# Kernel tuning notes

Measured on AMD Instinct MI355X. Metric: run time of the kernel, lower is better.

Reference implementation:

```python
import jax, jax.numpy as jnp
import numpy as np


def setup_inputs() -> dict:
    key = jax.random.key(0)
    ks = jax.random.split(key, 8)
    B, N, E, D, C = 64, 1024, 16384, 1024, 128
    x = jax.random.normal(ks[0], (B, D), dtype=jnp.float32)
    edge_index = jax.random.randint(ks[1], (2, E), 0, N, dtype=jnp.int64)
    W_emb = jax.random.normal(ks[2], (D, C), dtype=jnp.float32) * (2.0 / D) ** 0.5
    b_emb = jnp.zeros((C,), dtype=jnp.float32)
    W_conv = jax.random.normal(ks[3], (C, C), dtype=jnp.float32) * (2.0 / C) ** 0.5
    b_conv = jnp.zeros((C,), dtype=jnp.float32)
    W_cls = jax.random.normal(ks[4], (C, 1), dtype=jnp.float32) * (2.0 / C) ** 0.5
    b_cls = jnp.zeros((1,), dtype=jnp.float32)
    return {"x": x, "edge_index": edge_index, "W_emb": W_emb, "b_emb": b_emb,
            "W_conv": W_conv, "b_conv": b_conv, "W_cls": W_cls, "b_cls": b_cls,
            "n_nodes": N, "n_conv": 4}


def reference(x, edge_index, W_emb, b_emb, W_conv, b_conv, W_cls, b_cls, n_nodes, n_conv):
    B = x.shape[0]
    total = B * n_nodes
    # tile each flattened sample across all nodes of its graph copy  [B*N, D]
    x_batch = jnp.repeat(x.reshape(B, -1), n_nodes, axis=0)
    # batched edge index: disjoint union of B copies of the graph  [2, B*E]
    offs = (jnp.arange(B, dtype=edge_index.dtype) * n_nodes)[None, :, None]
    ei = (edge_index[:, None, :] + offs).reshape(2, -1)
    src, dst = ei[0], ei[1]
    # embedding: Linear + ReLU
    h = jax.nn.relu(x_batch @ W_emb + b_emb)
    # n_conv applications of the SAME GCNConv (no self loops, no normalization) + ReLU
    def conv(h, _):
        hw = h @ W_conv                                   # [B*N, C]
        agg = jax.ops.segment_sum(hw[src], dst, num_segments=total)
        return jax.nn.relu(agg + b_conv), None
    h, _ = jax.lax.scan(conv, h, None, length=n_conv)
    # node 0 of each graph copy, then classifier
    out = h[::n_nodes] @ W_cls + b_cls                    # [B, 1]
    return out
```

## Files before the change

kernel.cpp:

```cpp
#include <hip/hip_runtime.h>
#include <cstdint>
#include <cstddef>

constexpr int Bn = 64;
constexpr int Nn = 1024;
constexpr int Dn = 1024;
constexpr int Cn = 128;
constexpr int En = 16384;
constexpr int DMAX = 64;
constexpr int NB3 = 192;

typedef short s16x8 __attribute__((ext_vector_type(8)));
typedef float f32x4 __attribute__((ext_vector_type(4)));

__device__ __forceinline__ uint32_t f2bf(float f) {
    uint32_t u = __float_as_uint(f);
    return (u + 0x7fffu + ((u >> 16) & 1u)) >> 16;
}

__global__ __launch_bounds__(256) void k_prep(const float* __restrict__ x,
                                              const float* __restrict__ We,
                                              const float* __restrict__ Wc,
                                              const int* __restrict__ ei32,
                                              float* __restrict__ pws,
                                              unsigned short* __restrict__ Wt,
                                              unsigned int* __restrict__ epk,
                                              int* __restrict__ hists,
                                              int* __restrict__ f3,
                                              int* __restrict__ Mm,
                                              int* __restrict__ n3cur,
                                              int* __restrict__ meta) {
    int bid = blockIdx.x, tid = threadIdx.x;
    if (bid < 512) {
        __shared__ float sx[128];
        __shared__ float sp[256];
        int b = bid >> 3, q = bid & 7;
        int c = tid & 127, h = tid >> 7;
        if (tid < 128) sx[tid] = x[b * Dn + q * 128 + tid];
        __syncthreads();
        float acc = 0.f;
        int kl = h * 64;
        int d0 = q * 128 + kl;
#pragma unroll 8
        for (int i = 0; i < 64; ++i) acc += sx[kl + i] * We[(d0 + i) * Cn + c];
        sp[h * 128 + c] = acc;
        __syncthreads();
        if (h == 0) pws[(b * 8 + q) * Cn + c] = sp[c] + sp[128 + c];
    } else if (bid < 576) {
        int i = (bid - 512) * 256 + tid;
        int n = i >> 7, k = i & 127;
        Wt[i] = (unsigned short)f2bf(Wc[k * Cn + n]);
    } else if (bid < 592) {
        int hb = bid - 576;
        __shared__ int hloc[Nn];
        __shared__ int det;
#pragma unroll
        for (int r = 0; r < 4; ++r) hloc[r * 256 + tid] = 0;
        if (tid == 0) det = 0;
        __syncthreads();
        int base = hb * 1024;
        int hw = 0;
#pragma unroll
        for (int r = 0; r < 4; ++r) { int i = base + r * 256 + tid; hw |= ei32[2 * i + 1]; }
        if (hw) atomicOr(&det, 1);
        __syncthreads();
        bool i64 = (det == 0);
#pragma unroll
        for (int r = 0; r < 4; ++r) {
            int i = base + r * 256 + tid;
            int s, d;
            if (i64) {
                s = ((const int2*)ei32)[i].x & (Nn - 1);
                d = ((const int2*)ei32)[En + i].x & (Nn - 1);
            } else {
                s = ei32[i] & (Nn - 1);
                d = ei32[En + i] & (Nn - 1);
            }
            epk[i] = (unsigned)s | ((unsigned)d << 16);
            atomicAdd(&hloc[d], 1);
            if (d == 0) f3[s] = 1;
        }
        __syncthreads();
#pragma unroll
        for (int r = 0; r < 4; ++r) hists[hb * Nn + r * 256 + tid] = hloc[r * 256 + tid];
    } else if (bid < 596) {
        int4 z = {0, 0, 0, 0};
        int4* M4 = (int4*)Mm;
#pragma unroll
        for (int r = 0; r < 16; ++r) M4[(bid - 592) * 4096 + r * 256 + tid] = z;
    } else {
        int4 z = {0, 0, 0, 0};
        ((int4*)n3cur)[tid] = z;
        if (tid == 0) meta[4] = 0;
    }
}

__global__ __launch_bounds__(1024) void k_build(const int* __restrict__ hists,
                                                const unsigned int* __restrict__ epk,
                                                const int* __restrict__ f3,
                                                int* __restrict__ f2,
                                                int* __restrict__ Mm,
                                                int* __restrict__ n3cur,
                                                int* __restrict__ n3src,
                                                int* __restrict__ e0,
                                                int* __restrict__ L3,
                                                int* __restrict__ meta,
                                                const float* __restrict__ pws,
                                                const float* __restrict__ be,
                                                const float* __restrict__ Wc,
                                                float* __restrict__ g) {
    int bid = blockIdx.x, t = threadIdx.x;
    if (bid < 16) {
        __shared__ int sInd[Nn];
        int v = 0;
#pragma unroll
        for (int h = 0; h < 16; ++h) v += hists[h * Nn + t];
        sInd[t] = v;
        __syncthreads();
        unsigned e = epk[bid * 1024 + t];
        int s = e & 0xffff, d = e >> 16;
        int dd = sInd[s]; if (dd > DMAX - 1) dd = DMAX - 1;
        atomicAdd(&Mm[d * DMAX + dd], 1);
        if (f3[d] == 1) {
            f2[s] = 1;
            int p = atomicAdd(&n3cur[d], 1);
            if (p < NB3) n3src[d * NB3 + p] = s;
        }
        if (d == 0) {
            int p = atomicAdd(&meta[4], 1);
            if (p < 1024) e0[p] = s;
        }
    } else if (bid == 16) {
        __shared__ int c3;
        if (t == 0) c3 = 0;
        __syncthreads();
        if (f3[t] == 1) { int p = atomicAdd(&c3, 1); L3[p] = t; }
        __syncthreads();
        if (t == 0) meta[2] = c3;
    } else {
        __shared__ float se[8][Cn];
        int blk = bid - 17, bi = t >> 7, c = t & 127, b = blk * 8 + bi;
        float e4 = be[c];
#pragma unroll
        for (int q = 0; q < 8; ++q) e4 += pws[(b * 8 + q) * Cn + c];
        se[bi][c] = fmaxf(e4, 0.f);
        __syncthreads();
        float acc = 0.f;
#pragma unroll 8
        for (int k = 0; k < Cn; ++k) acc += se[bi][k] * Wc[k * Cn + c];
        g[b * Cn + c] = acc;
    }
}

constexpr int PAD = 136;
constexpr int PADR = 72;

__global__ __launch_bounds__(256, 4) void k_conv2M(const float* __restrict__ g,
                                                   float* __restrict__ h2,
                                                   const unsigned short* __restrict__ Wt,
                                                   const float* __restrict__ bc,
                                                   const int* __restrict__ Mm,
                                                   const int* __restrict__ f2) {
    int bidx = blockIdx.x;
    int tile0 = bidx >> 6, b = bidx & 63;
    __shared__ int sL2[Nn];
    __shared__ int sWs[4];
    __shared__ unsigned short sRt[128 * PADR];
    __shared__ unsigned short sMb[32 * PADR];
    __shared__ unsigned short sSb[32 * PAD];
    __shared__ int snode[32];
    int tid = threadIdx.x, lane = tid & 63, w = tid >> 6;
    int m = lane & 15, quad = lane >> 4;

    int n0 = tid * 4;
    int fl0 = (f2[n0] == 1), fl1 = (f2[n0 + 1] == 1), fl2 = (f2[n0 + 2] == 1), fl3 = (f2[n0 + 3] == 1);
    int c = fl0 + fl1 + fl2 + fl3;
    int inc = c;
    for (int off = 1; off < 64; off <<= 1) {
        int nv = __shfl_up(inc, off);
        if (lane >= off) inc += nv;
    }
    if (lane == 63) sWs[w] = inc;
    __syncthreads();
    int wbase = 0;
#pragma unroll
    for (int q = 0; q < 4; ++q) wbase += (q < w) ? sWs[q] : 0;
    int cnt2 = sWs[0] + sWs[1] + sWs[2] + sWs[3];
    int pos = wbase + inc - c;
    if (fl0) sL2[pos++] = n0;
    if (fl1) sL2[pos++] = n0 + 1;
    if (fl2) sL2[pos++] = n0 + 2;
    if (fl3) sL2[pos++] = n0 + 3;

    {
        int cc = tid & 127, dh = tid >> 7;
        float gc = g[b * Cn + cc], bcc = bc[cc];
#pragma unroll
        for (int d = dh * 32; d < dh * 32 + 32; ++d) {
            float r = fmaxf(fmaf((float)d, gc, bcc), 0.f);
            sRt[cc * PADR + d] = (unsigned short)f2bf(r);
        }
    }

    s16x8 bf0[4], bf1[4];
#pragma unroll
    for (int ks = 0; ks < 4; ++ks) {
        int ko = ks * 32 + quad * 8;
        bf0[ks] = *(const s16x8*)&Wt[(w * 32 + m) * Cn + ko];
        bf1[ks] = *(const s16x8*)&Wt[(w * 32 + 16 + m) * Cn + ko];
    }
    __syncthreads();

    for (int tile = tile0; tile * 32 < cnt2; tile += 8) {
        __syncthreads();
        if (tid < 32) {
            int ti = tile * 32 + tid;
            snode[tid] = (ti < cnt2) ? sL2[ti] : -1;
        }
        __syncthreads();
        {
            int row = tid >> 3, seg = tid & 7;
            int node = snode[row];
            unsigned short pk[8];
            if (node >= 0) {
                const int4* mp = (const int4*)&Mm[node * DMAX + seg * 8];
                int4 a = mp[0], bq = mp[1];
                pk[0] = (unsigned short)f2bf((float)a.x);
                pk[1] = (unsigned short)f2bf((float)a.y);
                pk[2] = (unsigned short)f2bf((float)a.z);
                pk[3] = (unsigned short)f2bf((float)a.w);
                pk[4] = (unsigned short)f2bf((float)bq.x);
                pk[5] = (unsigned short)f2bf((float)bq.y);
                pk[6] = (unsigned short)f2bf((float)bq.z);
                pk[7] = (unsigned short)f2bf((float)bq.w);
            } else {
#pragma unroll
                for (int i = 0; i < 8; ++i) pk[i] = 0;
            }
            *(uint4*)&sMb[row * PADR + seg * 8] = *(uint4*)pk;
        }
        __syncthreads();

        f32x4 acc1[2][2];
#pragma unroll
        for (int rt = 0; rt < 2; ++rt)
#pragma unroll
            for (int ct = 0; ct < 2; ++ct) acc1[rt][ct] = (f32x4){0.f, 0.f, 0.f, 0.f};
#pragma unroll
        for (int ks = 0; ks < 2; ++ks) {
            int ko = ks * 32 + quad * 8;
            s16x8 a0 = *(const s16x8*)&sMb[m * PADR + ko];
            s16x8 a1 = *(const s16x8*)&sMb[(16 + m) * PADR + ko];
            s16x8 r0 = *(const s16x8*)&sRt[(w * 32 + m) * PADR + ko];
            s16x8 r1 = *(const s16x8*)&sRt[(w * 32 + 16 + m) * PADR + ko];
            acc1[0][0] = __builtin_amdgcn_mfma_f32_16x16x32_bf16(a0, r0, acc1[0][0], 0, 0, 0);
            acc1[0][1] = __builtin_amdgcn_mfma_f32_16x16x32_bf16(a0, r1, acc1[0][1], 0, 0, 0);
            acc1[1][0] = __builtin_amdgcn_mfma_f32_16x16x32_bf16(a1, r0, acc1[1][0], 0, 0, 0);
            acc1[1][1] = __builtin_amdgcn_mfma_f32_16x16x32_bf16(a1, r1, acc1[1][1], 0, 0, 0);
        }
#pragma unroll
        for (int rt = 0; rt < 2; ++rt)
#pragma unroll
            for (int ct = 0; ct < 2; ++ct) {
                int col = w * 32 + ct * 16 + m;
#pragma unroll
                for (int reg = 0; reg < 4; ++reg) {
                    int row = rt * 16 + quad * 4 + reg;
                    sSb[row * PAD + col] = (unsigned short)f2bf(acc1[rt][ct][reg]);
                }
            }
        __syncthreads();

        f32x4 acc[2][2];
#pragma unroll
        for (int rt = 0; rt < 2; ++rt)
#pragma unroll
            for (int ct = 0; ct < 2; ++ct) acc[rt][ct] = (f32x4){0.f, 0.f, 0.f, 0.f};
#pragma unroll
        for (int ks = 0; ks < 4; ++ks) {
            int ko = ks * 32 + quad * 8;
            s16x8 a0 = *(const s16x8*)&sSb[(0 * 16 + m) * PAD + ko];
            s16x8 a1 = *(const s16x8*)&sSb[(1 * 16 + m) * PAD + ko];
            acc[0][0] = __builtin_amdgcn_mfma_f32_16x16x32_bf16(a0, bf0[ks], acc[0][0], 0, 0, 0);
            acc[0][1] = __builtin_amdgcn_mfma_f32_16x16x32_bf16(a0, bf1[ks], acc[0][1], 0, 0, 0);
            acc[1][0] = __builtin_amdgcn_mfma_f32_16x16x32_bf16(a1, bf0[ks], acc[1][0], 0, 0, 0);
            acc[1][1] = __builtin_amdgcn_mfma_f32_16x16x32_bf16(a1, bf1[ks], acc[1][1], 0, 0, 0);
        }

#pragma unroll
        for (int rt = 0; rt < 2; ++rt)
#pragma unroll
            for (int ct = 0; ct < 2; ++ct) {
                int col = w * 32 + ct * 16 + m;
                float bias = bc[col];
#pragma unroll
                for (int reg = 0; reg < 4; ++reg) {
                    int row = rt * 16 + quad * 4 + reg;
                    int node = snode[row];
                    if (node >= 0)
                        h2[((size_t)b * Nn + node) * Cn + col] = fmaxf(acc[rt][ct][reg] + bias, 0.f);
                }
            }
    }
}

__global__ __launch_bounds__(256) void k_conv34(const float* __restrict__ h2,
                                                const unsigned short* __restrict__ Wt,
                                                const float* __restrict__ bc,
                                                const int* __restrict__ L3,
                                                const int* __restrict__ meta,
                                                const int* __restrict__ n3cur,
                                                const int* __restrict__ n3src,
                                                const int* __restrict__ e0,
                                                const float* __restrict__ Wc,
                                                const float* __restrict__ Wcls,
                                                const float* __restrict__ bcls,
                                                float* __restrict__ out) {
    __shared__ unsigned short sSb[32 * PAD];
    __shared__ int sIdx[32][64];
    __shared__ float sH3[32][Cn];
    __shared__ short smap[Nn];
    __shared__ int snode[32], scnt[32];
    __shared__ float sAgg[8][Cn];
    __shared__ float sred[256];
    __shared__ int sI[256];
    int b = blockIdx.x, tid = threadIdx.x;
    int cnt3 = meta[2];
    int m0 = meta[4]; if (m0 > 1024) m0 = 1024;
    int lim = m0 < 256 ? m0 : 256;
    if (tid < lim) sI[tid] = e0[tid];

    int w = tid >> 6, lane = tid & 63, m = lane & 15, quad = lane >> 4;
    s16x8 bf0[4], bf1[4];
#pragma unroll
    for (int ks = 0; ks < 4; ++ks) {
        int ko = ks * 32 + quad * 8;
        bf0[ks] = *(const s16x8*)&Wt[(w * 32 + m) * Cn + ko];
        bf1[ks] = *(const s16x8*)&Wt[(w * 32 + 16 + m) * Cn + ko];
    }
    int c4 = tid & 31, u = tid >> 5;
    const float4* hb4 = (const float4*)(h2 + (size_t)b * (Nn * Cn));
    float4 aAgg = {0.f, 0.f, 0.f, 0.f};

    for (int tile = 0; tile * 32 < cnt3; ++tile) {
        __syncthreads();
#pragma unroll
        for (int r = 0; r < 4; ++r) smap[tid + 256 * r] = -1;
        if (tid < 32) {
            int ti = tile * 32 + tid;
            int node = (ti < cnt3) ? L3[ti] : -1;
            snode[tid] = node;
            int cnt = (node >= 0) ? n3cur[node] : 0;
            if (cnt > NB3) cnt = NB3;
            scnt[tid] = cnt;
        }
        __syncthreads();
        if (tid < 32 && snode[tid] >= 0) smap[snode[tid]] = (short)tid;
#pragma unroll
        for (int r = 0; r < 8; ++r) {
            int row = w * 8 + r;
            int cnt = scnt[row];
            if (lane < cnt && lane < 64) sIdx[row][lane] = n3src[snode[row] * NB3 + lane];
        }
        __syncthreads();

#pragma unroll
        for (int t0 = 0; t0 < 4; ++t0) {
            int row = u * 4 + t0;
            int cnt = scnt[row];
            float4 a = {0.f, 0.f, 0.f, 0.f};
            int jm = cnt < 64 ? cnt : 64;
            for (int j = 0; j < jm; ++j) {
                float4 v = hb4[sIdx[row][j] * 32 + c4];
                a.x += v.x; a.y += v.y; a.z += v.z; a.w += v.w;
            }
            for (int j = 64; j < cnt; ++j) {
                float4 v = hb4[n3src[snode[row] * NB3 + j] * 32 + c4];
                a.x += v.x; a.y += v.y; a.z += v.z; a.w += v.w;
            }
            uint2 pk;
            pk.x = f2bf(a.x) | (f2bf(a.y) << 16);
            pk.y = f2bf(a.z) | (f2bf(a.w) << 16);
            *(uint2*)&sSb[row * PAD + c4 * 4] = pk;
        }
        __syncthreads();

        f32x4 acc[2][2];
#pragma unroll
        for (int rt = 0; rt < 2; ++rt)
#pragma unroll
            for (int ct = 0; ct < 2; ++ct) acc[rt][ct] = (f32x4){0.f, 0.f, 0.f, 0.f};
#pragma unroll
        for (int ks = 0; ks < 4; ++ks) {
            int ko = ks * 32 + quad * 8;
            s16x8 a0 = *(const s16x8*)&sSb[(0 * 16 + m) * PAD + ko];
            s16x8 a1 = *(const s16x8*)&sSb[(1 * 16 + m) * PAD + ko];
            acc[0][0] = __builtin_amdgcn_mfma_f32_16x16x32_bf16(a0, bf0[ks], acc[0][0], 0, 0, 0);
            acc[0][1] = __builtin_amdgcn_mfma_f32_16x16x32_bf16(a0, bf1[ks], acc[0][1], 0, 0, 0);
            acc[1][0] = __builtin_amdgcn_mfma_f32_16x16x32_bf16(a1, bf0[ks], acc[1][0], 0, 0, 0);
            acc[1][1] = __builtin_amdgcn_mfma_f32_16x16x32_bf16(a1, bf1[ks], acc[1][1], 0, 0, 0);
        }

#pragma unroll
        for (int rt = 0; rt < 2; ++rt)
#pragma unroll
            for (int ct = 0; ct < 2; ++ct) {
                int col = w * 32 + ct * 16 + m;
                float bias = bc[col];
#pragma unroll
                for (int reg = 0; reg < 4; ++reg) {
                    int row = rt * 16 + quad * 4 + reg;
                    sH3[row][col] = fmaxf(acc[rt][ct][reg] + bias, 0.f);
                }
            }
        __syncthreads();

        for (int j = u; j < lim; j += 8) {
            int r2 = smap[sI[j]];
            if (r2 >= 0) {
                float4 v = *(const float4*)&sH3[r2][c4 * 4];
                aAgg.x += v.x; aAgg.y += v.y; aAgg.z += v.z; aAgg.w += v.w;
            }
        }
        for (int j = 256 + u; j < m0; j += 8) {
            int r2 = smap[e0[j]];
            if (r2 >= 0) {
                float4 v = *(const float4*)&sH3[r2][c4 * 4];
                aAgg.x += v.x; aAgg.y += v.y; aAgg.z += v.z; aAgg.w += v.w;
            }
        }
    }

    *(float4*)&sAgg[u][c4 * 4] = aAgg;
    __syncthreads();
    int c = tid & 127, half = tid >> 7;
    if (tid < 128) {
        float s = sAgg[0][c];
#pragma unroll
        for (int q2 = 1; q2 < 8; ++q2) s += sAgg[q2][c];
        sAgg[0][c] = s;
    }
    __syncthreads();
    float s = 0.f;
    int k0 = half * 64;
#pragma unroll 8
    for (int k = k0; k < k0 + 64; ++k) s += sAgg[0][k] * Wc[k * Cn + c];
    sred[tid] = s;
    __syncthreads();
    if (tid < 128) {
        float val = fmaxf(sred[c] + sred[128 + c] + bc[c], 0.f);
        sred[tid] = val * Wcls[c];
    }
    __syncthreads();
    for (int st = 64; st > 0; st >>= 1) {
        if (tid < st) sred[tid] += sred[tid + st];
        __syncthreads();
    }
    if (tid == 0) out[b] = sred[0] + bcls[0];
}

extern "C" void kernel_launch(void* const* d_in, const int* in_sizes, int n_in,
                              void* d_out, int out_size, void* d_ws, size_t ws_size,
                              hipStream_t stream) {
    const float* x    = (const float*)d_in[0];
    const int*   ei32 = (const int*)d_in[1];
    const float* We   = (const float*)d_in[2];
    const float* be   = (const float*)d_in[3];
    const float* Wc   = (const float*)d_in[4];
    const float* bc   = (const float*)d_in[5];
    const float* Wcls = (const float*)d_in[6];
    const float* bcls = (const float*)d_in[7];
    float* out = (float*)d_out;

    char* ws = (char*)d_ws;
    float*          g      = (float*)(ws + 0);
    int*            meta   = (int*)(ws + 32768);
    int*            e0     = (int*)(ws + 36864);
    int*            n3cur  = (int*)(ws + 40960);
    unsigned short* Wt     = (unsigned short*)(ws + 45056);
    float*          pws    = (float*)(ws + 77824);
    int*            f3     = (int*)(ws + 339968);
    int*            f2     = (int*)(ws + 344064);
    unsigned int*   epk    = (unsigned int*)(ws + 348160);
    int*            hists  = (int*)(ws + 413696);
    int*            Mm     = (int*)(ws + 479232);
    int*            n3src  = (int*)(ws + 741376);
    int*            L3     = (int*)(ws + 1527808);
    float*          h2full = (float*)(ws + 1531904);

    k_prep<<<597, 256, 0, stream>>>(x, We, Wc, ei32, pws, Wt, epk, hists, f3, Mm, n3cur, meta);
    k_build<<<25, 1024, 0, stream>>>(hists, epk, f3, f2, Mm, n3cur, n3src, e0, L3, meta,
                                     pws, be, Wc, g);
    k_conv2M<<<8 * Bn, 256, 0, stream>>>(g, h2full, Wt, bc, Mm, f2);
    k_conv34<<<Bn, 256, 0, stream>>>(h2full, Wt, bc, L3, meta, n3cur, n3src, e0,
                                     Wc, Wcls, bcls, out);
}
```

Measured before the change: 109.3 us.

## Fuse build, conv2 and conv3/4 kernels into one persistent kernel with global flags

Merges the graph-build, second-conv and final conv/classifier kernels into a single launch of 576 blocks. Blocks coordinate through global atomic counters and acquire spin-waits on a sync counter and per-batch h2 completion counters. Each conv2 block now recomputes its own embedding-times-W_conv vector, so the separate g stage is no longer needed. This removes two kernel launch boundaries and their drain gaps, but it relies on all 576 blocks being co-resident to avoid deadlock and adds spin-wait and fence overhead.

```diff
diff --git a/kernel.cpp b/kernel.cpp
--- a/kernel.cpp
+++ b/kernel.cpp
@@ -91,372 +91,404 @@
     } else {
         int4 z = {0, 0, 0, 0};
         ((int4*)n3cur)[tid] = z;
-        if (tid == 0) meta[4] = 0;
+        if (tid < 64) ((int4*)meta)[tid] = z;
     }
 }
 
-__global__ __launch_bounds__(1024) void k_build(const int* __restrict__ hists,
-                                                const unsigned int* __restrict__ epk,
-                                                const int* __restrict__ f3,
-                                                int* __restrict__ f2,
-                                                int* __restrict__ Mm,
-                                                int* __restrict__ n3cur,
-                                                int* __restrict__ n3src,
-                                                int* __restrict__ e0,
-                                                int* __restrict__ L3,
-                                                int* __restrict__ meta,
-                                                const float* __restrict__ pws,
-                                                const float* __restrict__ be,
-                                                const float* __restrict__ Wc,
-                                                float* __restrict__ g) {
-    int bid = blockIdx.x, t = threadIdx.x;
-    if (bid < 16) {
-        __shared__ int sInd[Nn];
-        int v = 0;
-#pragma unroll
-        for (int h = 0; h < 16; ++h) v += hists[h * Nn + t];
-        sInd[t] = v;
-        __syncthreads();
-        unsigned e = epk[bid * 1024 + t];
-        int s = e & 0xffff, d = e >> 16;
-        int dd = sInd[s]; if (dd > DMAX - 1) dd = DMAX - 1;
-        atomicAdd(&Mm[d * DMAX + dd], 1);
-        if (f3[d] == 1) {
-            f2[s] = 1;
-            int p = atomicAdd(&n3cur[d], 1);
-            if (p < NB3) n3src[d * NB3 + p] = s;
-        }
-        if (d == 0) {
-            int p = atomicAdd(&meta[4], 1);
-            if (p < 1024) e0[p] = s;
-        }
-    } else if (bid == 16) {
-        __shared__ int c3;
-        if (t == 0) c3 = 0;
-        __syncthreads();
-        if (f3[t] == 1) { int p = atomicAdd(&c3, 1); L3[p] = t; }
-        __syncthreads();
-        if (t == 0) meta[2] = c3;
-    } else {
-        __shared__ float se[8][Cn];
-        int blk = bid - 17, bi = t >> 7, c = t & 127, b = blk * 8 + bi;
-        float e4 = be[c];
-#pragma unroll
-        for (int q = 0; q < 8; ++q) e4 += pws[(b * 8 + q) * Cn + c];
-        se[bi][c] = fmaxf(e4, 0.f);
-        __syncthreads();
-        float acc = 0.f;
-#pragma unroll 8
-        for (int k = 0; k < Cn; ++k) acc += se[bi][k] * Wc[k * Cn + c];
-        g[b * Cn + c] = acc;
-    }
-}
-
 constexpr int PAD = 136;
 constexpr int PADR = 72;
 
-__global__ __launch_bounds__(256, 4) void k_conv2M(const float* __restrict__ g,
-                                                   float* __restrict__ h2,
-                                                   const unsigned short* __restrict__ Wt,
-                                                   const float* __restrict__ bc,
-                                                   const int* __restrict__ Mm,
-                                                   const int* __restrict__ f2) {
-    int bidx = blockIdx.x;
-    int tile0 = bidx >> 6, b = bidx & 63;
-    __shared__ int sL2[Nn];
-    __shared__ int sWs[4];
-    __shared__ unsigned short sRt[128 * PADR];
-    __shared__ unsigned short sMb[32 * PADR];
-    __shared__ unsigned short sSb[32 * PAD];
-    __shared__ int snode[32];
-    int tid = threadIdx.x, lane = tid & 63, w = tid >> 6;
-    int m = lane & 15, quad = lane >> 4;
-
-    int n0 = tid * 4;
-    int fl0 = (f2[n0] == 1), fl1 = (f2[n0 + 1] == 1), fl2 = (f2[n0 + 2] == 1), fl3 = (f2[n0 + 3] == 1);
-    int c = fl0 + fl1 + fl2 + fl3;
-    int inc = c;
-    for (int off = 1; off < 64; off <<= 1) {
-        int nv = __shfl_up(inc, off);
-        if (lane >= off) inc += nv;
-    }
-    if (lane == 63) sWs[w] = inc;
-    __syncthreads();
-    int wbase = 0;
-#pragma unroll
-    for (int q = 0; q < 4; ++q) wbase += (q < w) ? sWs[q] : 0;
-    int cnt2 = sWs[0] + sWs[1] + sWs[2] + sWs[3];
-    int pos = wbase + inc - c;
-    if (fl0) sL2[pos++] = n0;
-    if (fl1) sL2[pos++] = n0 + 1;
-    if (fl2) sL2[pos++] = n0 + 2;
-    if (fl3) sL2[pos++] = n0 + 3;
-
-    {
-        int cc = tid & 127, dh = tid >> 7;
-        float gc = g[b * Cn + cc], bcc = bc[cc];
-#pragma unroll
-        for (int d = dh * 32; d < dh * 32 + 32; ++d) {
-            float r = fmaxf(fmaf((float)d, gc, bcc), 0.f);
-            sRt[cc * PADR + d] = (unsigned short)f2bf(r);
-        }
-    }
-
-    s16x8 bf0[4], bf1[4];
-#pragma unroll
-    for (int ks = 0; ks < 4; ++ks) {
-        int ko = ks * 32 + quad * 8;
-        bf0[ks] = *(const s16x8*)&Wt[(w * 32 + m) * Cn + ko];
-        bf1[ks] = *(const s16x8*)&Wt[(w * 32 + 16 + m) * Cn + ko];
-    }
-    __syncthreads();
-
-    for (int tile = tile0; tile * 32 < cnt2; tile += 8) {
-        __syncthreads();
-        if (tid < 32) {
-            int ti = tile * 32 + tid;
-            snode[tid] = (ti < cnt2) ? sL2[ti] : -1;
+__global__ __launch_bounds__(256, 3) void k_fused(const float* __restrict__ pws,
+                                                  const float* __restrict__ be,
+                                                  const float* __restrict__ Wc,
+                                                  const float* __restrict__ bc,
+                                                  const unsigned short* __restrict__ Wt,
+                                                  const int* __restrict__ f3,
+                                                  int* __restrict__ f2,
+                                                  const unsigned int* __restrict__ epk,
+                                                  const int* __restrict__ hists,
+                                                  int* __restrict__ Mm,
+                                                  int* __restrict__ n3cur,
+                                                  int* __restrict__ n3src,
+                                                  int* __restrict__ e0,
+                                                  int* __restrict__ L3,
+                                                  int* __restrict__ meta,
+                                                  float* __restrict__ h2,
+                                                  const float* __restrict__ Wcls,
+                                                  const float* __restrict__ bcls,
+                                                  float* __restrict__ out) {
+    __shared__ char smem[43776];
+    __shared__ int sMisc[2];
+    int bid = blockIdx.x, tid = threadIdx.x;
+    int lane = tid & 63, w = tid >> 6, m = lane & 15, quad = lane >> 4;
+    int* sync0  = &meta[8];
+    int* h2done = &meta[64];
+
+    if (bid < 512) {
+        int tile0 = bid >> 6, b = bid & 63;
+        int*   shInt = (int*)smem;
+        int*   sWs   = (int*)(smem + 4096);
+        float* sE    = (float*)(smem + 4112);
+        float* sGp   = (float*)(smem + 4624);
+        float* sG    = (float*)(smem + 5648);
+        int*   snode = (int*)(smem + 6160);
+        unsigned short* sRt = (unsigned short*)(smem + 6400);
+        unsigned short* sMb = (unsigned short*)(smem + 24832);
+        unsigned short* sSb = (unsigned short*)(smem + 29440);
+
+        if (bid < 16) {
+            for (int i = tid; i < Nn; i += 256) {
+                int v = 0;
+#pragma unroll
+                for (int h = 0; h < 16; ++h) v += hists[h * Nn + i];
+                shInt[i] = v;
+            }
+            __syncthreads();
+#pragma unroll
+            for (int r = 0; r < 4; ++r) {
+                unsigned e = epk[bid * 1024 + r * 256 + tid];
+                int s = e & 0xffff, d = e >> 16;
+                int dd = shInt[s]; if (dd > DMAX - 1) dd = DMAX - 1;
+                atomicAdd(&Mm[d * DMAX + dd], 1);
+                if (f3[d] == 1) {
+                    f2[s] = 1;
+                    int p = atomicAdd(&n3cur[d], 1);
+                    if (p < NB3) n3src[d * NB3 + p] = s;
+                }
+                if (d == 0) {
+                    int p = atomicAdd(&meta[4], 1);
+                    if (p < 1024) e0[p] = s;
+                }
+            }
+            __threadfence();
+            __syncthreads();
+            if (tid == 0)
+                __hip_atomic_fetch_add(sync0, 1, __ATOMIC_RELEASE, __HIP_MEMORY_SCOPE_AGENT);
+            __syncthreads();
+        } else if (bid == 16) {
+            if (tid == 0) sMisc[0] = 0;
+            __syncthreads();
+            for (int i = tid; i < Nn; i += 256)
+                if (f3[i] == 1) { int p = atomicAdd(&sMisc[0], 1); L3[p] = i; }
+            __syncthreads();
+            if (tid == 0) meta[2] = sMisc[0];
+            __threadfence();
+            __syncthreads();
+            if (tid == 0)
+                __hip_atomic_fetch_add(sync0, 1, __ATOMIC_RELEASE, __HIP_MEMORY_SCOPE_AGENT);
+            __syncthreads();
+        }
+
+        int cc = tid & 127, half = tid >> 7;
+        if (half == 0) {
+            float e4 = be[cc];
+#pragma unroll
+            for (int q = 0; q < 8; ++q) e4 += pws[(b * 8 + q) * Cn + cc];
+            sE[cc] = fmaxf(e4, 0.f);
         }
         __syncthreads();
         {
-            int row = tid >> 3, seg = tid & 7;
-            int node = snode[row];
-            unsigned short pk[8];
-            if (node >= 0) {
-                const int4* mp = (const int4*)&Mm[node * DMAX + seg * 8];
-                int4 a = mp[0], bq = mp[1];
-                pk[0] = (unsigned short)f2bf((float)a.x);
-                pk[1] = (unsigned short)f2bf((float)a.y);
-                pk[2] = (unsigned short)f2bf((float)a.z);
-                pk[3] = (unsigned short)f2bf((float)a.w);
-                pk[4] = (unsigned short)f2bf((float)bq.x);
-                pk[5] = (unsigned short)f2bf((float)bq.y);
-                pk[6] = (unsigned short)f2bf((float)bq.z);
-                pk[7] = (unsigned short)f2bf((float)bq.w);
-            } else {
-#pragma unroll
-                for (int i = 0; i < 8; ++i) pk[i] = 0;
-            }
-            *(uint4*)&sMb[row * PADR + seg * 8] = *(uint4*)pk;
-        }
-        __syncthreads();
-
-        f32x4 acc1[2][2];
-#pragma unroll
-        for (int rt = 0; rt < 2; ++rt)
-#pragma unroll
-            for (int ct = 0; ct < 2; ++ct) acc1[rt][ct] = (f32x4){0.f, 0.f, 0.f, 0.f};
-#pragma unroll
-        for (int ks = 0; ks < 2; ++ks) {
-            int ko = ks * 32 + quad * 8;
-            s16x8 a0 = *(const s16x8*)&sMb[m * PADR + ko];
-            s16x8 a1 = *(const s16x8*)&sMb[(16 + m) * PADR + ko];
-            s16x8 r0 = *(const s16x8*)&sRt[(w * 32 + m) * PADR + ko];
-            s16x8 r1 = *(const s16x8*)&sRt[(w * 32 + 16 + m) * PADR + ko];
-            acc1[0][0] = __builtin_amdgcn_mfma_f32_16x16x32_bf16(a0, r0, acc1[0][0], 0, 0, 0);
-            acc1[0][1] = __builtin_amdgcn_mfma_f32_16x16x32_bf16(a0, r1, acc1[0][1], 0, 0, 0);
-            acc1[1][0] = __builtin_amdgcn_mfma_f32_16x16x32_bf16(a1, r0, acc1[1][0], 0, 0, 0);
-            acc1[1][1] = __builtin_amdgcn_mfma_f32_16x16x32_bf16(a1, r1, acc1[1][1], 0, 0, 0);
-        }
-#pragma unroll
-        for (int rt = 0; rt < 2; ++rt)
-#pragma unroll
-            for (int ct = 0; ct < 2; ++ct) {
-                int col = w * 32 + ct * 16 + m;
-#pragma unroll
-                for (int reg = 0; reg < 4; ++reg) {
-                    int row = rt * 16 + quad * 4 + reg;
-                    sSb[row * PAD + col] = (unsigned short)f2bf(acc1[rt][ct][reg]);
-                }
-            }
-        __syncthreads();
-
-        f32x4 acc[2][2];
-#pragma unroll
-        for (int rt = 0; rt < 2; ++rt)
-#pragma unroll
-            for (int ct = 0; ct < 2; ++ct) acc[rt][ct] = (f32x4){0.f, 0.f, 0.f, 0.f};
+            float gp = 0.f;
+            int k0 = half * 64;
+#pragma unroll 8
+            for (int k = k0; k < k0 + 64; ++k) gp += sE[k] * Wc[k * Cn + cc];
+            sGp[half * 128 + cc] = gp;
+        }
+        __syncthreads();
+        if (half == 0) sG[cc] = sGp[cc] + sGp[128 + cc];
+        __syncthreads();
+
+        {
+            float gc = sG[cc], bcc = bc[cc];
+#pragma unroll
+            for (int d = half * 32; d < half * 32 + 32; ++d) {
+                float r = fmaxf(fmaf((float)d, gc, bcc), 0.f);
+                sRt[cc * PADR + d] = (unsigned short)f2bf(r);
+            }
+        }
+
+        s16x8 bf0[4], bf1[4];
 #pragma unroll
         for (int ks = 0; ks < 4; ++ks) {
             int ko = ks * 32 + quad * 8;
-            s16x8 a0 = *(const s16x8*)&sSb[(0 * 16 + m) * PAD + ko];
-            s16x8 a1 = *(const s16x8*)&sSb[(1 * 16 + m) * PAD + ko];
-            acc[0][0] = __builtin_amdgcn_mfma_f32_16x16x32_bf16(a0, bf0[ks], acc[0][0], 0, 0, 0);
-            acc[0][1] = __builtin_amdgcn_mfma_f32_16x16x32_bf16(a0, bf1[ks], acc[0][1], 0, 0, 0);
-            acc[1][0] = __builtin_amdgcn_mfma_f32_16x16x32_bf16(a1, bf0[ks], acc[1][0], 0, 0, 0);
-            acc[1][1] = __builtin_amdgcn_mfma_f32_16x16x32_bf16(a1, bf1[ks], acc[1][1], 0, 0, 0);
-        }
-
-#pragma unroll
-        for (int rt = 0; rt < 2; ++rt)
-#pragma unroll
-            for (int ct = 0; ct < 2; ++ct) {
-                int col = w * 32 + ct * 16 + m;
-                float bias = bc[col];
-#pragma unroll
-                for (int reg = 0; reg < 4; ++reg) {
-                    int row = rt * 16 + quad * 4 + reg;
-                    int node = snode[row];
-                    if (node >= 0)
-                        h2[((size_t)b * Nn + node) * Cn + col] = fmaxf(acc[rt][ct][reg] + bias, 0.f);
-                }
-            }
-    }
-}
-
-__global__ __launch_bounds__(256) void k_conv34(const float* __restrict__ h2,
-                                                const unsigned short* __restrict__ Wt,
-                                                const float* __restrict__ bc,
-                                                const int* __restrict__ L3,
-                                                const int* __restrict__ meta,
-                                                const int* __restrict__ n3cur,
-                                                const int* __restrict__ n3src,
-                                                const int* __restrict__ e0,
-                                                const float* __restrict__ Wc,
-                                                const float* __restrict__ Wcls,
-                                                const float* __restrict__ bcls,
-                                                float* __restrict__ out) {
-    __shared__ unsigned short sSb[32 * PAD];
-    __shared__ int sIdx[32][64];
-    __shared__ float sH3[32][Cn];
-    __shared__ short smap[Nn];
-    __shared__ int snode[32], scnt[32];
-    __shared__ float sAgg[8][Cn];
-    __shared__ float sred[256];
-    __shared__ int sI[256];
-    int b = blockIdx.x, tid = threadIdx.x;
-    int cnt3 = meta[2];
-    int m0 = meta[4]; if (m0 > 1024) m0 = 1024;
-    int lim = m0 < 256 ? m0 : 256;
-    if (tid < lim) sI[tid] = e0[tid];
-
-    int w = tid >> 6, lane = tid & 63, m = lane & 15, quad = lane >> 4;
-    s16x8 bf0[4], bf1[4];
-#pragma unroll
-    for (int ks = 0; ks < 4; ++ks) {
-        int ko = ks * 32 + quad * 8;
-        bf0[ks] = *(const s16x8*)&Wt[(w * 32 + m) * Cn + ko];
-        bf1[ks] = *(const s16x8*)&Wt[(w * 32 + 16 + m) * Cn + ko];
-    }
-    int c4 = tid & 31, u = tid >> 5;
-    const float4* hb4 = (const float4*)(h2 + (size_t)b * (Nn * Cn));
-    float4 aAgg = {0.f, 0.f, 0.f, 0.f};
-
-    for (int tile = 0; tile * 32 < cnt3; ++tile) {
-        __syncthreads();
-#pragma unroll
-        for (int r = 0; r < 4; ++r) smap[tid + 256 * r] = -1;
-        if (tid < 32) {
-            int ti = tile * 32 + tid;
-            int node = (ti < cnt3) ? L3[ti] : -1;
-            snode[tid] = node;
-            int cnt = (node >= 0) ? n3cur[node] : 0;
-            if (cnt > NB3) cnt = NB3;
-            scnt[tid] = cnt;
-        }
-        __syncthreads();
-        if (tid < 32 && snode[tid] >= 0) smap[snode[tid]] = (short)tid;
-#pragma unroll
-        for (int r = 0; r < 8; ++r) {
-            int row = w * 8 + r;
-            int cnt = scnt[row];
-            if (lane < cnt && lane < 64) sIdx[row][lane] = n3src[snode[row] * NB3 + lane];
-        }
-        __syncthreads();
-
-#pragma unroll
-        for (int t0 = 0; t0 < 4; ++t0) {
-            int row = u * 4 + t0;
-            int cnt = scnt[row];
-            float4 a = {0.f, 0.f, 0.f, 0.f};
-            int jm = cnt < 64 ? cnt : 64;
-            for (int j = 0; j < jm; ++j) {
-                float4 v = hb4[sIdx[row][j] * 32 + c4];
-                a.x += v.x; a.y += v.y; a.z += v.z; a.w += v.w;
-            }
-            for (int j = 64; j < cnt; ++j) {
-                float4 v = hb4[n3src[snode[row] * NB3 + j] * 32 + c4];
-                a.x += v.x; a.y += v.y; a.z += v.z; a.w += v.w;
-            }
-            uint2 pk;
-            pk.x = f2bf(a.x) | (f2bf(a.y) << 16);
-            pk.y = f2bf(a.z) | (f2bf(a.w) << 16);
-            *(uint2*)&sSb[row * PAD + c4 * 4] = pk;
-        }
-        __syncthreads();
-
-        f32x4 acc[2][2];
-#pragma unroll
-        for (int rt = 0; rt < 2; ++rt)
-#pragma unroll
-            for (int ct = 0; ct < 2; ++ct) acc[rt][ct] = (f32x4){0.f, 0.f, 0.f, 0.f};
+            bf0[ks] = *(const s16x8*)&Wt[(w * 32 + m) * Cn + ko];
+            bf1[ks] = *(const s16x8*)&Wt[(w * 32 + 16 + m) * Cn + ko];
+        }
+
+        if (tid == 0) {
+            while (__hip_atomic_load(sync0, __ATOMIC_ACQUIRE, __HIP_MEMORY_SCOPE_AGENT) < 17)
+                __builtin_amdgcn_s_sleep(2);
+        }
+        __syncthreads();
+
+        int n0 = tid * 4;
+        int fl0 = (f2[n0] == 1), fl1 = (f2[n0 + 1] == 1),
+            fl2 = (f2[n0 + 2] == 1), fl3 = (f2[n0 + 3] == 1);
+        int cflags = fl0 + fl1 + fl2 + fl3;
+        int inc = cflags;
+        for (int off = 1; off < 64; off <<= 1) {
+            int nv = __shfl_up(inc, off);
+            if (lane >= off) inc += nv;
+        }
+        if (lane == 63) sWs[w] = inc;
+        __syncthreads();
+        int wbase = 0;
+#pragma unroll
+        for (int q = 0; q < 4; ++q) wbase += (q < w) ? sWs[q] : 0;
+        int cnt2 = sWs[0] + sWs[1] + sWs[2] + sWs[3];
+        int pos = wbase + inc - cflags;
+        if (fl0) shInt[pos++] = n0;
+        if (fl1) shInt[pos++] = n0 + 1;
+        if (fl2) shInt[pos++] = n0 + 2;
+        if (fl3) shInt[pos++] = n0 + 3;
+
+        for (int tile = tile0; tile * 32 < cnt2; tile += 8) {
+            __syncthreads();
+            if (tid < 32) {
+                int ti = tile * 32 + tid;
+                snode[tid] = (ti < cnt2) ? shInt[ti] : -1;
+            }
+            __syncthreads();
+            {
+                int row = tid >> 3, seg = tid & 7;
+                int node = snode[row];
+                unsigned short pk[8];
+                if (node >= 0) {
+                    const int4* mp = (const int4*)&Mm[node * DMAX + seg * 8];
+                    int4 a = mp[0], bq = mp[1];
+                    pk[0] = (unsigned short)f2bf((float)a.x);
+                    pk[1] = (unsigned short)f2bf((float)a.y);
+                    pk[2] = (unsigned short)f2bf((float)a.z);
+                    pk[3] = (unsigned short)f2bf((float)a.w);
+                    pk[4] = (unsigned short)f2bf((float)bq.x);
+                    pk[5] = (unsigned short)f2bf((float)bq.y);
+                    pk[6] = (unsigned short)f2bf((float)bq.z);
+                    pk[7] = (unsigned short)f2bf((float)bq.w);
+                } else {
+#pragma unroll
+                    for (int i = 0; i < 8; ++i) pk[i] = 0;
+                }
+                *(uint4*)&sMb[row * PADR + seg * 8] = *(uint4*)pk;
+            }
+            __syncthreads();
+
+            f32x4 acc1[2][2];
+#pragma unroll
+            for (int rt = 0; rt < 2; ++rt)
+#pragma unroll
+                for (int ct = 0; ct < 2; ++ct) acc1[rt][ct] = (f32x4){0.f, 0.f, 0.f, 0.f};
+#pragma unroll
+            for (int ks = 0; ks < 2; ++ks) {
+                int ko = ks * 32 + quad * 8;
+                s16x8 a0 = *(const s16x8*)&sMb[m * PADR + ko];
+                s16x8 a1 = *(const s16x8*)&sMb[(16 + m) * PADR + ko];
+                s16x8 r0 = *(const s16x8*)&sRt[(w * 32 + m) * PADR + ko];
+                s16x8 r1 = *(const s16x8*)&sRt[(w * 32 + 16 + m) * PADR + ko];
+                acc1[0][0] = __builtin_amdgcn_mfma_f32_16x16x32_bf16(a0, r0, acc1[0][0], 0, 0, 0);
+                acc1[0][1] = __builtin_amdgcn_mfma_f32_16x16x32_bf16(a0, r1, acc1[0][1], 0, 0, 0);
+                acc1[1][0] = __builtin_amdgcn_mfma_f32_16x16x32_bf16(a1, r0, acc1[1][0], 0, 0, 0);
+                acc1[1][1] = __builtin_amdgcn_mfma_f32_16x16x32_bf16(a1, r1, acc1[1][1], 0, 0, 0);
+            }
+#pragma unroll
+            for (int rt = 0; rt < 2; ++rt)
+#pragma unroll
+                for (int ct = 0; ct < 2; ++ct) {
+                    int col = w * 32 + ct * 16 + m;
+#pragma unroll
+                    for (int reg = 0; reg < 4; ++reg) {
+                        int row = rt * 16 + quad * 4 + reg;
+                        sSb[row * PAD + col] = (unsigned short)f2bf(acc1[rt][ct][reg]);
+                    }
+                }
+            __syncthreads();
+
+            f32x4 acc[2][2];
+#pragma unroll
+            for (int rt = 0; rt < 2; ++rt)
+#pragma unroll
+                for (int ct = 0; ct < 2; ++ct) acc[rt][ct] = (f32x4){0.f, 0.f, 0.f, 0.f};
+#pragma unroll
+            for (int ks = 0; ks < 4; ++ks) {
+                int ko = ks * 32 + quad * 8;
+                s16x8 a0 = *(const s16x8*)&sSb[(0 * 16 + m) * PAD + ko];
+                s16x8 a1 = *(const s16x8*)&sSb[(1 * 16 + m) * PAD + ko];
+                acc[0][0] = __builtin_amdgcn_mfma_f32_16x16x32_bf16(a0, bf0[ks], acc[0][0], 0, 0, 0);
+                acc[0][1] = __builtin_amdgcn_mfma_f32_16x16x32_bf16(a0, bf1[ks], acc[0][1], 0, 0, 0);
+                acc[1][0] = __builtin_amdgcn_mfma_f32_16x16x32_bf16(a1, bf0[ks], acc[1][0], 0, 0, 0);
+                acc[1][1] = __builtin_amdgcn_mfma_f32_16x16x32_bf16(a1, bf1[ks], acc[1][1], 0, 0, 0);
+            }
+
+#pragma unroll
+            for (int rt = 0; rt < 2; ++rt)
+#pragma unroll
+                for (int ct = 0; ct < 2; ++ct) {
+                    int col = w * 32 + ct * 16 + m;
+                    float bias = bc[col];
+#pragma unroll
+                    for (int reg = 0; reg < 4; ++reg) {
+                        int row = rt * 16 + quad * 4 + reg;
+                        int node = snode[row];
+                        if (node >= 0)
+                            h2[((size_t)b * Nn + node) * Cn + col] = fmaxf(acc[rt][ct][reg] + bias, 0.f);
+                    }
+                }
+        }
+
+        __threadfence();
+        __syncthreads();
+        if (tid == 0)
+            __hip_atomic_fetch_add(&h2done[b], 1, __ATOMIC_RELEASE, __HIP_MEMORY_SCOPE_AGENT);
+    } else {
+        int b = bid - 512;
+        unsigned short* sSb = (unsigned short*)smem;
+        int (*sIdx)[64]     = (int(*)[64])(smem + 8704);
+        float (*sH3)[Cn]    = (float(*)[Cn])(smem + 16896);
+        short* smap         = (short*)(smem + 33280);
+        int*   snode        = (int*)(smem + 35328);
+        int*   scnt         = (int*)(smem + 35456);
+        float (*sAgg)[Cn]   = (float(*)[Cn])(smem + 35584);
+        float* sred         = (float*)(smem + 39680);
+        int*   sI           = (int*)(smem + 40704);
+
+        s16x8 bf0[4], bf1[4];
 #pragma unroll
         for (int ks = 0; ks < 4; ++ks) {
             int ko = ks * 32 + quad * 8;
-            s16x8 a0 = *(const s16x8*)&sSb[(0 * 16 + m) * PAD + ko];
-            s16x8 a1 = *(const s16x8*)&sSb[(1 * 16 + m) * PAD + ko];
-            acc[0][0] = __builtin_amdgcn_mfma_f32_16x16x32_bf16(a0, bf0[ks], acc[0][0], 0, 0, 0);
-            acc[0][1] = __builtin_amdgcn_mfma_f32_16x16x32_bf16(a0, bf1[ks], acc[0][1], 0, 0, 0);
-            acc[1][0] = __builtin_amdgcn_mfma_f32_16x16x32_bf16(a1, bf0[ks], acc[1][0], 0, 0, 0);
-            acc[1][1] = __builtin_amdgcn_mfma_f32_16x16x32_bf16(a1, bf1[ks], acc[1][1], 0, 0, 0);
-        }
-
-#pragma unroll
-        for (int rt = 0; rt < 2; ++rt)
-#pragma unroll
-            for (int ct = 0; ct < 2; ++ct) {
-                int col = w * 32 + ct * 16 + m;
-                float bias = bc[col];
-#pragma unroll
-                for (int reg = 0; reg < 4; ++reg) {
-                    int row = rt * 16 + quad * 4 + reg;
-                    sH3[row][col] = fmaxf(acc[rt][ct][reg] + bias, 0.f);
-                }
-            }
-        __syncthreads();
-
-        for (int j = u; j < lim; j += 8) {
-            int r2 = smap[sI[j]];
-            if (r2 >= 0) {
-                float4 v = *(const float4*)&sH3[r2][c4 * 4];
-                aAgg.x += v.x; aAgg.y += v.y; aAgg.z += v.z; aAgg.w += v.w;
-            }
-        }
-        for (int j = 256 + u; j < m0; j += 8) {
-            int r2 = smap[e0[j]];
-            if (r2 >= 0) {
-                float4 v = *(const float4*)&sH3[r2][c4 * 4];
-                aAgg.x += v.x; aAgg.y += v.y; aAgg.z += v.z; aAgg.w += v.w;
-            }
-        }
+            bf0[ks] = *(const s16x8*)&Wt[(w * 32 + m) * Cn + ko];
+            bf1[ks] = *(const s16x8*)&Wt[(w * 32 + 16 + m) * Cn + ko];
+        }
+
+        if (tid == 0) {
+            while (__hip_atomic_load(&h2done[b], __ATOMIC_ACQUIRE, __HIP_MEMORY_SCOPE_AGENT) < 8)
+                __builtin_amdgcn_s_sleep(2);
+        }
+        __syncthreads();
+
+        int cnt3 = meta[2];
+        int m0 = meta[4]; if (m0 > 1024) m0 = 1024;
+        int lim = m0 < 256 ? m0 : 256;
+        if (tid < lim) sI[tid] = e0[tid];
+
+        int c4 = tid & 31, u = tid >> 5;
+        const float4* hb4 = (const float4*)(h2 + (size_t)b * (Nn * Cn));
+        float4 aAgg = {0.f, 0.f, 0.f, 0.f};
+
+        for (int tile = 0; tile * 32 < cnt3; ++tile) {
+            __syncthreads();
+#pragma unroll
+            for (int r = 0; r < 4; ++r) smap[tid + 256 * r] = -1;
+            if (tid < 32) {
+                int ti = tile * 32 + tid;
+                int node = (ti < cnt3) ? L3[ti] : -1;
+                snode[tid] = node;
+                int cnt = (node >= 0) ? n3cur[node] : 0;
+                if (cnt > NB3) cnt = NB3;
+                scnt[tid] = cnt;
+            }
+            __syncthreads();
+            if (tid < 32 && snode[tid] >= 0) smap[snode[tid]] = (short)tid;
+#pragma unroll
+            for (int r = 0; r < 8; ++r) {
+                int row = w * 8 + r;
+                int cnt = scnt[row];
+                if (lane < cnt && lane < 64) sIdx[row][lane] = n3src[snode[row] * NB3 + lane];
+            }
+            __syncthreads();
+
+#pragma unroll
+            for (int t0 = 0; t0 < 4; ++t0) {
+                int row = u * 4 + t0;
+                int cnt = scnt[row];
+                float4 a = {0.f, 0.f, 0.f, 0.f};
+                int jm = cnt < 64 ? cnt : 64;
+                for (int j = 0; j < jm; ++j) {
+                    float4 v = hb4[sIdx[row][j] * 32 + c4];
+                    a.x += v.x; a.y += v.y; a.z += v.z; a.w += v.w;
+                }
+                for (int j = 64; j < cnt; ++j) {
+                    float4 v = hb4[n3src[snode[row] * NB3 + j] * 32 + c4];
+                    a.x += v.x; a.y += v.y; a.z += v.z; a.w += v.w;
+                }
+                uint2 pk;
+                pk.x = f2bf(a.x) | (f2bf(a.y) << 16);
+                pk.y = f2bf(a.z) | (f2bf(a.w) << 16);
+                *(uint2*)&sSb[row * PAD + c4 * 4] = pk;
+            }
+            __syncthreads();
+
+            f32x4 acc[2][2];
+#pragma unroll
+            for (int rt = 0; rt < 2; ++rt)
+#pragma unroll
+                for (int ct = 0; ct < 2; ++ct) acc[rt][ct] = (f32x4){0.f, 0.f, 0.f, 0.f};
+#pragma unroll
+            for (int ks = 0; ks < 4; ++ks) {
+                int ko = ks * 32 + quad * 8;
+                s16x8 a0 = *(const s16x8*)&sSb[(0 * 16 + m) * PAD + ko];
+                s16x8 a1 = *(const s16x8*)&sSb[(1 * 16 + m) * PAD + ko];
+                acc[0][0] = __builtin_amdgcn_mfma_f32_16x16x32_bf16(a0, bf0[ks], acc[0][0], 0, 0, 0);
+                acc[0][1] = __builtin_amdgcn_mfma_f32_16x16x32_bf16(a0, bf1[ks], acc[0][1], 0, 0, 0);
+                acc[1][0] = __builtin_amdgcn_mfma_f32_16x16x32_bf16(a1, bf0[ks], acc[1][0], 0, 0, 0);
+                acc[1][1] = __builtin_amdgcn_mfma_f32_16x16x32_bf16(a1, bf1[ks], acc[1][1], 0, 0, 0);
+            }
+
+#pragma unroll
+            for (int rt = 0; rt < 2; ++rt)
+#pragma unroll
+                for (int ct = 0; ct < 2; ++ct) {
+                    int col = w * 32 + ct * 16 + m;
+                    float bias = bc[col];
+#pragma unroll
+                    for (int reg = 0; reg < 4; ++reg) {
+                        int row = rt * 16 + quad * 4 + reg;
+                        sH3[row][col] = fmaxf(acc[rt][ct][reg] + bias, 0.f);
+                    }
+                }
+            __syncthreads();
+
+            for (int j = u; j < lim; j += 8) {
+                int r2 = smap[sI[j]];
+                if (r2 >= 0) {
+                    float4 v = *(const float4*)&sH3[r2][c4 * 4];
+                    aAgg.x += v.x; aAgg.y += v.y; aAgg.z += v.z; aAgg.w += v.w;
+                }
+            }
+            for (int j = 256 + u; j < m0; j += 8) {
+                int r2 = smap[e0[j]];
+                if (r2 >= 0) {
+                    float4 v = *(const float4*)&sH3[r2][c4 * 4];
+                    aAgg.x += v.x; aAgg.y += v.y; aAgg.z += v.z; aAgg.w += v.w;
+                }
+            }
+        }
+
+        *(float4*)&sAgg[u][c4 * 4] = aAgg;
+        __syncthreads();
+        int c = tid & 127, half = tid >> 7;
+        if (tid < 128) {
+            float s = sAgg[0][c];
+#pragma unroll
+            for (int q2 = 1; q2 < 8; ++q2) s += sAgg[q2][c];
+            sAgg[0][c] = s;
+        }
+        __syncthreads();
+        float s = 0.f;
+        int k0 = half * 64;
+#pragma unroll 8
+        for (int k = k0; k < k0 + 64; ++k) s += sAgg[0][k] * Wc[k * Cn + c];
+        sred[tid] = s;
+        __syncthreads();
+        if (tid < 128) {
+            float val = fmaxf(sred[c] + sred[128 + c] + bc[c], 0.f);
+            sred[tid] = val * Wcls[c];
+        }
+        __syncthreads();
+        for (int st = 64; st > 0; st >>= 1) {
+            if (tid < st) sred[tid] += sred[tid + st];
+            __syncthreads();
+        }
+        if (tid == 0) out[b] = sred[0] + bcls[0];
     }
-
-    *(float4*)&sAgg[u][c4 * 4] = aAgg;
-    __syncthreads();
-    int c = tid & 127, half = tid >> 7;
-    if (tid < 128) {
-        float s = sAgg[0][c];
-#pragma unroll
-        for (int q2 = 1; q2 < 8; ++q2) s += sAgg[q2][c];
-        sAgg[0][c] = s;
-    }
-    __syncthreads();
-    float s = 0.f;
-    int k0 = half * 64;
-#pragma unroll 8
-    for (int k = k0; k < k0 + 64; ++k) s += sAgg[0][k] * Wc[k * Cn + c];
-    sred[tid] = s;
-    __syncthreads();
-    if (tid < 128) {
-        float val = fmaxf(sred[c] + sred[128 + c] + bc[c], 0.f);
-        sred[tid] = val * Wcls[c];
-    }
-    __syncthreads();
-    for (int st = 64; st > 0; st >>= 1) {
-        if (tid < st) sred[tid] += sred[tid + st];
-        __syncthreads();
-    }
-    if (tid == 0) out[b] = sred[0] + bcls[0];
 }
 
 extern "C" void kernel_launch(void* const* d_in, const int* in_sizes, int n_in,
@@ -473,7 +505,6 @@
     float* out = (float*)d_out;
 
     char* ws = (char*)d_ws;
-    float*          g      = (float*)(ws + 0);
     int*            meta   = (int*)(ws + 32768);
     int*            e0     = (int*)(ws + 36864);
     int*            n3cur  = (int*)(ws + 40960);
@@ -489,9 +520,7 @@
     float*          h2full = (float*)(ws + 1531904);
 
     k_prep<<<597, 256, 0, stream>>>(x, We, Wc, ei32, pws, Wt, epk, hists, f3, Mm, n3cur, meta);
-    k_build<<<25, 1024, 0, stream>>>(hists, epk, f3, f2, Mm, n3cur, n3src, e0, L3, meta,
-                                     pws, be, Wc, g);
-    k_conv2M<<<8 * Bn, 256, 0, stream>>>(g, h2full, Wt, bc, Mm, f2);
-    k_conv34<<<Bn, 256, 0, stream>>>(h2full, Wt, bc, L3, meta, n3cur, n3src, e0,
-                                     Wc, Wcls, bcls, out);
+    k_fused<<<576, 256, 0, stream>>>(pws, be, Wc, bc, Wt, f3, f2, epk, hists,
+                                     Mm, n3cur, n3src, e0, L3, meta, h2full,
+                                     Wcls, bcls, out);
 }
```

Result: slower. 245.4 us (+124.5%).
